# Performance work log

Hardware: AMD Instinct MI355X
Metric: run time of the kernel (lower is better)

The kernel has to match this reference:

```python
import jax, jax.numpy as jnp
import numpy as np


def spline_conv(x, src, dst, u, Wk, Wroot, bias, num_nodes):
    # Linear B-spline basis for dim=1, kernel_size=2, degree=1: [(1-u), u]
    # Transform at node level first (cheap GEMM), then gather/blend per edge.
    h0 = x @ Wk[0]           # [N, out]
    h1 = x @ Wk[1]           # [N, out]
    w1 = u[:, 0]             # [E]
    w0 = 1.0 - w1
    msg = w0[:, None] * h0[src] + w1[:, None] * h1[src]   # [E, out]
    agg = jax.ops.segment_sum(msg, dst, num_segments=num_nodes)
    deg = jax.ops.segment_sum(jnp.ones_like(w1), dst, num_segments=num_nodes)
    agg = agg / jnp.maximum(deg, 1.0)[:, None]             # aggr='mean'
    return agg + x @ Wroot + bias


def setup_inputs() -> dict:
    key = jax.random.key(0)
    k = jax.random.split(key, 10)
    N, F_IN, HID, C, E = 100000, 128, 16, 10, 1600000
    x = jax.random.normal(k[0], (N, F_IN), dtype=jnp.float32)
    edge_index = jax.random.randint(k[1], (2, E), 0, N, dtype=jnp.int64)
    edge_attr = jax.random.uniform(k[2], (E, 1), dtype=jnp.float32)
    s1 = 1.0 / np.sqrt(F_IN)
    s2 = 1.0 / np.sqrt(HID)
    W1 = jax.random.uniform(k[3], (2, F_IN, HID), jnp.float32, -s1, s1)
    root1 = jax.random.uniform(k[4], (F_IN, HID), jnp.float32, -s1, s1)
    b1 = jax.random.uniform(k[5], (HID,), jnp.float32, -s1, s1)
    W2 = jax.random.uniform(k[6], (2, HID, C), jnp.float32, -s2, s2)
    root2 = jax.random.uniform(k[7], (HID, C), jnp.float32, -s2, s2)
    b2 = jax.random.uniform(k[8], (C,), jnp.float32, -s2, s2)
    return {"x": x, "edge_index": edge_index, "edge_attr": edge_attr,
            "W1": W1, "root1": root1, "b1": b1,
            "W2": W2, "root2": root2, "b2": b2}


def reference(x, edge_index, edge_attr, W1, root1, b1, W2, root2, b2):
    N = x.shape[0]
    src, dst = edge_index[0], edge_index[1]
    # dropout is identity in eval mode
    h = spline_conv(x, src, dst, edge_attr, W1, root1, b1, N)
    h = jax.nn.elu(h)
    out = spline_conv(h, src, dst, edge_attr, W2, root2, b2, N)
    return out
```

## Files before the change

### kernel.cpp

```cpp
#include <hip/hip_runtime.h>
#include <math.h>


#define SHIFT    7
#define BNODES   128
#define NBUK_MAX 800
#define CAP      2432
#define CHUNK    4096

__device__ __forceinline__ unsigned short f2bf(float f) {
    unsigned int u = __float_as_uint(f);
    u += 0x7FFF + ((u >> 16) & 1);
    return (unsigned short)(u >> 16);
}


__device__ __forceinline__ void gemm_part(
    float* __restrict__ Ws, int gb, int tid,
    const float* __restrict__ x, const float* __restrict__ W1,
    const float* __restrict__ root1, unsigned int* __restrict__ h01i,
    float* __restrict__ xr, int N)
{
    for (int idx = tid; idx < 128 * 48; idx += 256) {
        int k = idx / 48, j = idx % 48;
        int grp = j >> 3, t = j & 7;
        float v;
        switch (grp) {
            case 0: v = W1[k * 16 + t];            break;
            case 1: v = W1[2048 + k * 16 + t];     break;
            case 2: v = root1[k * 16 + t];         break;
            case 3: v = W1[k * 16 + 8 + t];        break;
            case 4: v = W1[2048 + k * 16 + 8 + t]; break;
            default: v = root1[k * 16 + 8 + t];    break;
        }
        Ws[idx] = v;
    }
    __syncthreads();
    int nl   = tid >> 1;
    int half = tid & 1;
    int n = gb * 128 + nl;
    if (n >= N) return;

    float acc[24];
#pragma unroll
    for (int j = 0; j < 24; ++j) acc[j] = 0.f;

    const float4* xrow = (const float4*)(x + (size_t)n * 128);
    const float4* wbase = (const float4*)(Ws + half * 24);
#pragma unroll 4
    for (int k4 = 0; k4 < 32; ++k4) {
        float4 xv = xrow[k4];
        float xs[4] = {xv.x, xv.y, xv.z, xv.w};
#pragma unroll
        for (int kk = 0; kk < 4; ++kk) {
            float xk = xs[kk];
            const float4* w4 = wbase + ((k4 * 4 + kk) * 48) / 4;
#pragma unroll
            for (int q = 0; q < 6; ++q) {
                float4 wv = w4[q];
                acc[q * 4 + 0] += xk * wv.x;
                acc[q * 4 + 1] += xk * wv.y;
                acc[q * 4 + 2] += xk * wv.z;
                acc[q * 4 + 3] += xk * wv.w;
            }
        }
    }
    int cb = half * 8;
#pragma unroll
    for (int t = 0; t < 8; ++t)
        h01i[(size_t)n * 16 + cb + t] =
            (unsigned int)f2bf(acc[t]) | ((unsigned int)f2bf(acc[8 + t]) << 16);
#pragma unroll
    for (int t = 0; t < 8; ++t)
        xr[(size_t)n * 16 + cb + t] = acc[16 + t];
}

__device__ __forceinline__ void bin_part(
    int* __restrict__ smem, int bb, int tid,
    const int* __restrict__ ei, const float* __restrict__ ea,
    int* __restrict__ gcur, int2* __restrict__ staging, int E, int nbuk)
{
    int* bcnt  = smem;
    int* gbase = bcnt + NBUK_MAX;
    for (int i = tid; i < nbuk; i += 256) bcnt[i] = 0;
    __syncthreads();

    int base = bb * CHUNK;
    int lrank[16];
#pragma unroll
    for (int i = 0; i < 16; ++i) {
        int e = base + i * 256 + tid;
        lrank[i] = 0;
        if (e < E) lrank[i] = atomicAdd(&bcnt[ei[E + e] >> SHIFT], 1);
    }
    __syncthreads();
    for (int b = tid; b < nbuk; b += 256) {
        int c = bcnt[b];
        gbase[b] = c ? atomicAdd(&gcur[b], c) : 0;
    }
    __syncthreads();
#pragma unroll
    for (int i = 0; i < 16; ++i) {
        int e = base + i * 256 + tid;
        if (e < E) {
            int s = ei[e];
            int d = ei[E + e];
            int b = d >> SHIFT;
            int p = gbase[b] + lrank[i];
            if (p < CAP)
                staging[(size_t)b * CAP + p] =
                    make_int2(s | ((d & (BNODES - 1)) << 17), __float_as_int(ea[e]));
        }
    }
}

__global__ __launch_bounds__(256, 4) void phase1_kernel(
    const float* __restrict__ x, const float* __restrict__ W1,
    const float* __restrict__ root1, unsigned int* __restrict__ h01i,
    float* __restrict__ xr,
    const int* __restrict__ ei, const float* __restrict__ ea,
    int* __restrict__ gcur, int2* __restrict__ staging,
    int N, int E, int nbuk, int gemmBlocks, int binBlocks)
{
    __shared__ float smem[128 * 48];
    int tid = threadIdx.x;
    int bid = blockIdx.x;
    int sub = bid >> 1;
    if ((bid & 1) == 0) {
        if (sub < gemmBlocks)
            gemm_part(smem, sub, tid, x, W1, root1, h01i, xr, N);
    } else {
        if (sub < binBlocks)
            bin_part((int*)smem, sub, tid, ei, ea, gcur, staging, E, nbuk);
    }
}

__global__ __launch_bounds__(256) void csr_build_kernel(
    int2* __restrict__ staging, const int* __restrict__ gcur,
    int* __restrict__ roff, int* __restrict__ cnt, int N)
{
    __shared__ int2 rin[CAP];
    __shared__ int2 rout[CAP];
    __shared__ int hist[BNODES];
    __shared__ int sscan[BNODES];
    __shared__ int wcur[BNODES];
    int tid = threadIdx.x;
    int b = blockIdx.x;
    int m = gcur[b];
    if (m > CAP) m = CAP;
    int2* sp = staging + (size_t)b * CAP;

    if (tid < BNODES) { hist[tid] = 0; wcur[tid] = 0; }
    __syncthreads();
    for (int k = tid; k < m; k += 256) {
        int2 r = sp[k];
        rin[k] = r;
        atomicAdd(&hist[r.x >> 17], 1);
    }
    __syncthreads();
    if (tid < BNODES) sscan[tid] = hist[tid];
    __syncthreads();
    for (int off = 1; off < BNODES; off <<= 1) {
        int t = (tid < BNODES && tid >= off) ? sscan[tid - off] : 0;
        __syncthreads();
        if (tid < BNODES) sscan[tid] += t;
        __syncthreads();
    }
    for (int k = tid; k < m; k += 256) {
        int2 r = rin[k];
        int dl = r.x >> 17;
        int pos = (sscan[dl] - hist[dl]) + atomicAdd(&wcur[dl], 1);
        rout[pos] = make_int2(r.x & 0x1FFFF, r.y);
    }
    __syncthreads();
    for (int k = tid; k < m; k += 256) sp[k] = rout[k];
    if (tid < BNODES) {
        int n = b * BNODES + tid;
        if (n < N) {
            roff[n] = b * CAP + (sscan[tid] - hist[tid]);
            cnt[n]  = hist[tid];
        }
    }
}

__global__ __launch_bounds__(256) void gather1f_kernel(
    const int2* __restrict__ staging, const int* __restrict__ roff,
    const int* __restrict__ cnt, const unsigned int* __restrict__ h01i,
    const float* __restrict__ xr, const float* __restrict__ b1,
    const float* __restrict__ root2, const float* __restrict__ b2,
    unsigned short* __restrict__ hb, float* __restrict__ hrb, int N)
{
    __shared__ float r2s[160];
    __shared__ float b1s[16];
    __shared__ float b2s[10];
    int tid = threadIdx.x;
    if (tid < 160) r2s[tid] = root2[tid];
    if (tid < 16)  b1s[tid] = b1[tid];
    if (tid < 10)  b2s[tid] = b2[tid];
    __syncthreads();
    int t = blockIdx.x * 256 + tid;
    int n = t >> 4;
    int c = t & 15;
    if (n >= N) return;
    int start = roff[n];
    int m = cnt[n];
    float acc = 0.f;
#pragma unroll 2
    for (int k = 0; k < m; ++k) {
        int2 r = staging[(size_t)start + k];
        float w = __int_as_float(r.y);
        unsigned int v = h01i[(size_t)r.x * 16 + c];
        float a  = __uint_as_float(v << 16);
        float bb = __uint_as_float(v & 0xFFFF0000u);
        acc += a + w * (bb - a);
    }
    float invd = 1.0f / fmaxf((float)m, 1.0f);
    float hv = acc * invd + xr[(size_t)n * 16 + c] + b1s[c];
    hv = hv > 0.f ? hv : expm1f(hv);
    hb[(size_t)n * 16 + c] = f2bf(hv);

    float r[10];
#pragma unroll
    for (int j = 0; j < 10; ++j) r[j] = hv * r2s[c * 10 + j];
#pragma unroll
    for (int off = 1; off < 16; off <<= 1) {
#pragma unroll
        for (int j = 0; j < 10; ++j) r[j] += __shfl_xor(r[j], off);
    }
    if (c == 0) {
        float* hp = hrb + (size_t)n * 10;
#pragma unroll
        for (int j = 0; j < 10; ++j) hp[j] = r[j] + b2s[j];
    }
}

__global__ __launch_bounds__(256) void gather2f_kernel(
    const int2* __restrict__ staging, const int* __restrict__ roff,
    const int* __restrict__ cnt, const unsigned short* __restrict__ hb,
    const float* __restrict__ hrb, const float* __restrict__ W2,
    float* __restrict__ out, int N)
{
    __shared__ float w2s[320];
    int tid = threadIdx.x;
    for (int idx = tid; idx < 320; idx += 256) w2s[idx] = W2[idx];
    __syncthreads();
    int t = blockIdx.x * 256 + tid;
    int n = t >> 4;
    int c = t & 15;
    if (n >= N) return;
    int start = roff[n];
    int m = cnt[n];
    float p = 0.f, q = 0.f;
#pragma unroll 2
    for (int k = 0; k < m; ++k) {
        int2 r = staging[(size_t)start + k];
        float w = __int_as_float(r.y);
        float v = __uint_as_float(((unsigned int)hb[(size_t)r.x * 16 + c]) << 16);
        p += (1.f - w) * v;
        q += w * v;
    }
    float invd = 1.0f / fmaxf((float)m, 1.0f);
    float o[10];
#pragma unroll
    for (int j = 0; j < 10; ++j)
        o[j] = p * w2s[c * 10 + j] + q * w2s[160 + c * 10 + j];
#pragma unroll
    for (int off = 1; off < 16; off <<= 1) {
#pragma unroll
        for (int j = 0; j < 10; ++j) o[j] += __shfl_xor(o[j], off);
    }
    if (c == 0) {
        float* op = out + (size_t)n * 10;
        const float* hp = hrb + (size_t)n * 10;
#pragma unroll
        for (int j = 0; j < 10; ++j) op[j] = o[j] * invd + hp[j];
    }
}

extern "C" void kernel_launch(void* const* d_in, const int* in_sizes, int n_in,
                              void* d_out, int out_size, void* d_ws, size_t ws_size,
                              hipStream_t stream)
{
    const float* x     = (const float*)d_in[0];
    const int*   ei    = (const int*)d_in[1];
    const float* ea    = (const float*)d_in[2];
    const float* W1    = (const float*)d_in[3];
    const float* root1 = (const float*)d_in[4];
    const float* b1    = (const float*)d_in[5];
    const float* W2    = (const float*)d_in[6];
    const float* root2 = (const float*)d_in[7];
    const float* b2    = (const float*)d_in[8];
    float* out = (float*)d_out;

    int N = in_sizes[0] / 128;
    int E = in_sizes[2];
    int nbuk = (N + BNODES - 1) / BNODES;

    char* ws = (char*)d_ws;
    int2*  staging = (int2*)ws;
    unsigned int* h01i = (unsigned int*)(ws + (size_t)nbuk * CAP * 8);
    float* xr    = (float*)(h01i + (size_t)N * 16);
    float* hrb   = xr + (size_t)N * 16;
    unsigned short* hb = (unsigned short*)(hrb + (size_t)N * 10);
    int*   cnt   = (int*)(hb + (size_t)N * 16);
    int*   roff  = cnt + N;
    int*   gcur  = roff + N;

    int nb_e16 = (N * 16 + 255) / 256;
    int gemmBlocks = (N + 127) / 128;
    int binBlocks  = (E + CHUNK - 1) / CHUNK;
    int mixBlocks  = 2 * ((gemmBlocks > binBlocks) ? gemmBlocks : binBlocks);

    hipMemsetAsync(gcur, 0, (size_t)nbuk * sizeof(int), stream);

    phase1_kernel   <<<mixBlocks, 256, 0, stream>>>(
        x, W1, root1, h01i, xr, ei, ea, gcur, staging, N, E, nbuk,
        gemmBlocks, binBlocks);
    csr_build_kernel<<<nbuk, 256, 0, stream>>>(staging, gcur, roff, cnt, N);
    gather1f_kernel <<<nb_e16, 256, 0, stream>>>(staging, roff, cnt, h01i, xr,
                                                 b1, root2, b2, hb, hrb, N);
    gather2f_kernel <<<nb_e16, 256, 0, stream>>>(staging, roff, cnt, hb, hrb,
                                                 W2, out, N);
}
```

Baseline: 148.5 us.

## Pack CSR records to 32-bit with quantized weights and tile GEMM through LDS

The CSR records shrink from an int2 (index plus fp32 weight) to one 32-bit word: a 17-bit source index and a 15-bit fixed-point edge weight. This halves the record traffic in both gather kernels, and their unroll factor rises to 4. The layer-1 GEMM is also restructured: it stages 32-node tiles of x in LDS with padding, has 8 threads per node each compute 6 outputs, and writes results back through LDS for coalesced stores. The change adds quantization error to the edge weights, and more grid blocks plus a larger LDS footprint lower the occupancy hint from 4 to 3.

```diff
diff --git a/kernel.cpp b/kernel.cpp
--- a/kernel.cpp
+++ b/kernel.cpp
@@ -7,6 +7,8 @@
 #define NBUK_MAX 800
 #define CAP      2432
 #define CHUNK    4096
+#define GTN      32
+#define XPITCH   132
 
 __device__ __forceinline__ unsigned short f2bf(float f) {
     unsigned int u = __float_as_uint(f);
@@ -16,63 +18,65 @@
 
 
 __device__ __forceinline__ void gemm_part(
-    float* __restrict__ Ws, int gb, int tid,
+    float* __restrict__ smem, int gb, int tid,
     const float* __restrict__ x, const float* __restrict__ W1,
     const float* __restrict__ root1, unsigned int* __restrict__ h01i,
     float* __restrict__ xr, int N)
 {
+    float* xls = smem;
+    float* Ws  = smem + GTN * XPITCH;
     for (int idx = tid; idx < 128 * 48; idx += 256) {
         int k = idx / 48, j = idx % 48;
-        int grp = j >> 3, t = j & 7;
-        float v;
-        switch (grp) {
-            case 0: v = W1[k * 16 + t];            break;
-            case 1: v = W1[2048 + k * 16 + t];     break;
-            case 2: v = root1[k * 16 + t];         break;
-            case 3: v = W1[k * 16 + 8 + t];        break;
-            case 4: v = W1[2048 + k * 16 + 8 + t]; break;
-            default: v = root1[k * 16 + 8 + t];    break;
-        }
+        float v = (j < 16) ? W1[k * 16 + j]
+                : (j < 32) ? W1[2048 + k * 16 + (j - 16)]
+                           : root1[k * 16 + (j - 32)];
         Ws[idx] = v;
     }
-    __syncthreads();
-    int nl   = tid >> 1;
-    int half = tid & 1;
-    int n = gb * 128 + nl;
-    if (n >= N) return;
-
-    float acc[24];
-#pragma unroll
-    for (int j = 0; j < 24; ++j) acc[j] = 0.f;
-
-    const float4* xrow = (const float4*)(x + (size_t)n * 128);
-    const float4* wbase = (const float4*)(Ws + half * 24);
+    int node0 = gb * GTN;
+    for (int f = tid; f < GTN * 32; f += 256) {
+        int n = f >> 5, k4 = f & 31;
+        float4 v = make_float4(0.f, 0.f, 0.f, 0.f);
+        if (node0 + n < N)
+            v = ((const float4*)(x + (size_t)(node0 + n) * 128))[k4];
+        *(float4*)(xls + n * XPITCH + k4 * 4) = v;
+    }
+    __syncthreads();
+
+    int n = tid >> 3;
+    int q = tid & 7;
+    float acc[6] = {0.f, 0.f, 0.f, 0.f, 0.f, 0.f};
+    const float* wq = Ws + q * 6;
 #pragma unroll 4
     for (int k4 = 0; k4 < 32; ++k4) {
-        float4 xv = xrow[k4];
+        float4 xv = *(const float4*)(xls + n * XPITCH + k4 * 4);
         float xs[4] = {xv.x, xv.y, xv.z, xv.w};
 #pragma unroll
         for (int kk = 0; kk < 4; ++kk) {
+            const float* wr = wq + (k4 * 4 + kk) * 48;
             float xk = xs[kk];
-            const float4* w4 = wbase + ((k4 * 4 + kk) * 48) / 4;
-#pragma unroll
-            for (int q = 0; q < 6; ++q) {
-                float4 wv = w4[q];
-                acc[q * 4 + 0] += xk * wv.x;
-                acc[q * 4 + 1] += xk * wv.y;
-                acc[q * 4 + 2] += xk * wv.z;
-                acc[q * 4 + 3] += xk * wv.w;
-            }
+            acc[0] += xk * wr[0]; acc[1] += xk * wr[1];
+            acc[2] += xk * wr[2]; acc[3] += xk * wr[3];
+            acc[4] += xk * wr[4]; acc[5] += xk * wr[5];
         }
     }
-    int cb = half * 8;
-#pragma unroll
-    for (int t = 0; t < 8; ++t)
-        h01i[(size_t)n * 16 + cb + t] =
-            (unsigned int)f2bf(acc[t]) | ((unsigned int)f2bf(acc[8 + t]) << 16);
-#pragma unroll
-    for (int t = 0; t < 8; ++t)
-        xr[(size_t)n * 16 + cb + t] = acc[16 + t];
+    __syncthreads();
+    float* out = xls;
+    *(float2*)(out + n * 48 + q * 6)     = make_float2(acc[0], acc[1]);
+    *(float2*)(out + n * 48 + q * 6 + 2) = make_float2(acc[2], acc[3]);
+    *(float2*)(out + n * 48 + q * 6 + 4) = make_float2(acc[4], acc[5]);
+    __syncthreads();
+    for (int f = tid; f < GTN * 32; f += 256) {
+        int nn = f >> 5, c = f & 31;
+        int gnn = node0 + nn;
+        if (gnn >= N) continue;
+        if (c < 16) {
+            unsigned int lo = f2bf(out[nn * 48 + c]);
+            unsigned int hi = f2bf(out[nn * 48 + 16 + c]);
+            h01i[(size_t)gnn * 16 + c] = lo | (hi << 16);
+        } else {
+            xr[(size_t)gnn * 16 + (c - 16)] = out[nn * 48 + 32 + (c - 16)];
+        }
+    }
 }
 
 __device__ __forceinline__ void bin_part(
@@ -114,7 +118,7 @@
     }
 }
 
-__global__ __launch_bounds__(256, 4) void phase1_kernel(
+__global__ __launch_bounds__(256, 3) void phase1_kernel(
     const float* __restrict__ x, const float* __restrict__ W1,
     const float* __restrict__ root1, unsigned int* __restrict__ h01i,
     float* __restrict__ xr,
@@ -122,7 +126,7 @@
     int* __restrict__ gcur, int2* __restrict__ staging,
     int N, int E, int nbuk, int gemmBlocks, int binBlocks)
 {
-    __shared__ float smem[128 * 48];
+    __shared__ float smem[GTN * XPITCH + 128 * 48];
     int tid = threadIdx.x;
     int bid = blockIdx.x;
     int sub = bid >> 1;
@@ -140,7 +144,7 @@
     int* __restrict__ roff, int* __restrict__ cnt, int N)
 {
     __shared__ int2 rin[CAP];
-    __shared__ int2 rout[CAP];
+    __shared__ unsigned int rout[CAP];
     __shared__ int hist[BNODES];
     __shared__ int sscan[BNODES];
     __shared__ int wcur[BNODES];
@@ -170,21 +174,25 @@
         int2 r = rin[k];
         int dl = r.x >> 17;
         int pos = (sscan[dl] - hist[dl]) + atomicAdd(&wcur[dl], 1);
-        rout[pos] = make_int2(r.x & 0x1FFFF, r.y);
-    }
-    __syncthreads();
-    for (int k = tid; k < m; k += 256) sp[k] = rout[k];
+        float w = __int_as_float(r.y);
+        int wq = (int)(w * 32768.0f + 0.5f);
+        if (wq > 32767) wq = 32767;
+        rout[pos] = (unsigned int)(r.x & 0x1FFFF) | ((unsigned int)wq << 17);
+    }
+    __syncthreads();
+    unsigned int* sp32 = (unsigned int*)sp;
+    for (int k = tid; k < m; k += 256) sp32[k] = rout[k];
     if (tid < BNODES) {
         int n = b * BNODES + tid;
         if (n < N) {
-            roff[n] = b * CAP + (sscan[tid] - hist[tid]);
+            roff[n] = b * (CAP * 2) + (sscan[tid] - hist[tid]);
             cnt[n]  = hist[tid];
         }
     }
 }
 
 __global__ __launch_bounds__(256) void gather1f_kernel(
-    const int2* __restrict__ staging, const int* __restrict__ roff,
+    const unsigned int* __restrict__ staging, const int* __restrict__ roff,
     const int* __restrict__ cnt, const unsigned int* __restrict__ h01i,
     const float* __restrict__ xr, const float* __restrict__ b1,
     const float* __restrict__ root2, const float* __restrict__ b2,
@@ -205,11 +213,11 @@
     int start = roff[n];
     int m = cnt[n];
     float acc = 0.f;
-#pragma unroll 2
+#pragma unroll 4
     for (int k = 0; k < m; ++k) {
-        int2 r = staging[(size_t)start + k];
-        float w = __int_as_float(r.y);
-        unsigned int v = h01i[(size_t)r.x * 16 + c];
+        unsigned int rec = staging[(size_t)start + k];
+        float w = (float)(rec >> 17) * (1.0f / 32768.0f);
+        unsigned int v = h01i[(size_t)(rec & 0x1FFFF) * 16 + c];
         float a  = __uint_as_float(v << 16);
         float bb = __uint_as_float(v & 0xFFFF0000u);
         acc += a + w * (bb - a);
@@ -235,7 +243,7 @@
 }
 
 __global__ __launch_bounds__(256) void gather2f_kernel(
-    const int2* __restrict__ staging, const int* __restrict__ roff,
+    const unsigned int* __restrict__ staging, const int* __restrict__ roff,
     const int* __restrict__ cnt, const unsigned short* __restrict__ hb,
     const float* __restrict__ hrb, const float* __restrict__ W2,
     float* __restrict__ out, int N)
@@ -251,11 +259,11 @@
     int start = roff[n];
     int m = cnt[n];
     float p = 0.f, q = 0.f;
-#pragma unroll 2
+#pragma unroll 4
     for (int k = 0; k < m; ++k) {
-        int2 r = staging[(size_t)start + k];
-        float w = __int_as_float(r.y);
-        float v = __uint_as_float(((unsigned int)hb[(size_t)r.x * 16 + c]) << 16);
+        unsigned int rec = staging[(size_t)start + k];
+        float w = (float)(rec >> 17) * (1.0f / 32768.0f);
+        float v = __uint_as_float(((unsigned int)hb[(size_t)(rec & 0x1FFFF) * 16 + c]) << 16);
         p += (1.f - w) * v;
         q += w * v;
     }
@@ -307,7 +315,7 @@
     int*   gcur  = roff + N;
 
     int nb_e16 = (N * 16 + 255) / 256;
-    int gemmBlocks = (N + 127) / 128;
+    int gemmBlocks = (N + GTN - 1) / GTN;
     int binBlocks  = (E + CHUNK - 1) / CHUNK;
     int mixBlocks  = 2 * ((gemmBlocks > binBlocks) ? gemmBlocks : binBlocks);
 
@@ -317,8 +325,10 @@
         x, W1, root1, h01i, xr, ei, ea, gcur, staging, N, E, nbuk,
         gemmBlocks, binBlocks);
     csr_build_kernel<<<nbuk, 256, 0, stream>>>(staging, gcur, roff, cnt, N);
-    gather1f_kernel <<<nb_e16, 256, 0, stream>>>(staging, roff, cnt, h01i, xr,
+    gather1f_kernel <<<nb_e16, 256, 0, stream>>>((const unsigned int*)staging,
+                                                 roff, cnt, h01i, xr,
                                                  b1, root2, b2, hb, hrb, N);
-    gather2f_kernel <<<nb_e16, 256, 0, stream>>>(staging, roff, cnt, hb, hrb,
+    gather2f_kernel <<<nb_e16, 256, 0, stream>>>((const unsigned int*)staging,
+                                                 roff, cnt, hb, hrb,
                                                  W2, out, N);
 }
```

Measured after the change: 173.7 us. +16.9%, slower.
